# Optimization experiments

Measured on AMD Instinct MI355X. Metric: run time of the kernel, lower is better.

Reference implementation:

```python
import jax, jax.numpy as jnp
import numpy as np

SHAPE = (16, 1, 64, 128, 128)  # volume exactly equals the NCC window [64,128,128]
WIN_SIZE = 64.0 * 128.0 * 128.0


def setup_inputs() -> dict:
    key = jax.random.key(0)
    k1, k2, k3, k4 = jax.random.split(key, 4)
    out = jax.random.uniform(k1, SHAPE, dtype=jnp.float32)
    y_pred = jax.random.uniform(k2, SHAPE, dtype=jnp.float32)
    out_ccl = jax.random.randint(k3, SHAPE, 0, 2, dtype=jnp.int32)
    y_ccl = jax.random.randint(k4, SHAPE, 0, 2, dtype=jnp.int32)
    return {"out": out, "y_pred": y_pred, "out_ccl": out_ccl, "y_ccl": y_ccl}


def reference(out, y_pred, out_ccl, y_ccl):
    I, J = out, y_pred
    # masks at full resolution
    mask_I = jnp.where((out < 0.247) & (out_ccl > 0), 0.0, 1.0).astype(I.dtype)
    mask_J = jnp.where((y_pred < 0.247) & (y_ccl > 0), 0.0, 1.0).astype(J.dtype)

    # conv3d with an all-ones [64,128,128] kernel, stride 1, pad 0 over a
    # 64x128x128 volume == global sum per volume (output spatial dims are 1).
    ax = (2, 3, 4)
    I_sum = jnp.sum(I, axis=ax, keepdims=True)          # [B,1,1,1,1]
    J_sum = jnp.sum(J, axis=ax, keepdims=True)
    I2_sum = jnp.sum(I * I, axis=ax, keepdims=True)
    J2_sum = jnp.sum(J * J, axis=ax, keepdims=True)
    IJ_sum = jnp.sum(I * J, axis=ax, keepdims=True)

    u_I = I_sum / WIN_SIZE
    u_J = J_sum / WIN_SIZE
    cross = IJ_sum - u_J * I_sum - u_I * J_sum + u_I * u_J * WIN_SIZE
    I_var = I2_sum - 2.0 * u_I * I_sum + u_I * u_I * WIN_SIZE
    J_var = J2_sum - 2.0 * u_J * J_sum + u_J * u_J * WIN_SIZE
    cc = cross * cross / (I_var * J_var + 1e-5)         # [B,1,1,1,1]

    # broadcast per-volume cc against full-resolution masks, then mean
    return jnp.mean(-cc * mask_J * mask_I)
```

## Files before the change

### kernel.cpp

```cpp
#include <hip/hip_runtime.h>


#define NB   16
#define VOL  (64 * 128 * 128)
#define BPB  256
#define TPB  256
#define EPT  16

__device__ __forceinline__ double wave_reduce(double v) {
    #pragma unroll
    for (int off = 32; off > 0; off >>= 1) v += __shfl_down(v, off, 64);
    return v;
}

__global__ __launch_bounds__(TPB) void ncc_partial(
    const float* __restrict__ I, const float* __restrict__ J,
    const int* __restrict__ CI, const int* __restrict__ CJ,
    double* __restrict__ part)
{
    const int b = blockIdx.y;
    const size_t base = (size_t)b * VOL + (size_t)blockIdx.x * (TPB * EPT);
    const int tid = threadIdx.x;

    const float4* I4 = reinterpret_cast<const float4*>(I + base);
    const float4* J4 = reinterpret_cast<const float4*>(J + base);
    const int4*   C4 = reinterpret_cast<const int4*>(CI + base);
    const int4*   D4 = reinterpret_cast<const int4*>(CJ + base);

    double sI = 0.0, sJ = 0.0, sI2 = 0.0, sJ2 = 0.0, sIJ = 0.0;
    int cnt = 0;

    #pragma unroll
    for (int k = 0; k < EPT / 4; ++k) {
        const int idx = tid + k * TPB;
        float4 iv = I4[idx];
        float4 jv = J4[idx];
        int4   cv = C4[idx];
        int4   dv = D4[idx];

        float fi[4] = {iv.x, iv.y, iv.z, iv.w};
        float fj[4] = {jv.x, jv.y, jv.z, jv.w};
        int   ki[4] = {cv.x, cv.y, cv.z, cv.w};
        int   kj[4] = {dv.x, dv.y, dv.z, dv.w};

        #pragma unroll
        for (int e = 0; e < 4; ++e) {
            double di = (double)fi[e];
            double dj = (double)fj[e];
            sI += di;
            sJ += dj;
            sI2 = fma(di, di, sI2);
            sJ2 = fma(dj, dj, sJ2);
            sIJ = fma(di, dj, sIJ);
            bool zI = (di < 0.247) && (ki[e] > 0);
            bool zJ = (dj < 0.247) && (kj[e] > 0);
            cnt += (!zI && !zJ) ? 1 : 0;
        }
    }

    double v[6] = {sI, sJ, sI2, sJ2, sIJ, (double)cnt};
    #pragma unroll
    for (int q = 0; q < 6; ++q) v[q] = wave_reduce(v[q]);

    __shared__ double sh[TPB / 64][6];
    const int wave = tid >> 6, lane = tid & 63;
    if (lane == 0) {
        #pragma unroll
        for (int q = 0; q < 6; ++q) sh[wave][q] = v[q];
    }
    __syncthreads();

    if (tid == 0) {
        double o[6] = {0, 0, 0, 0, 0, 0};
        for (int w = 0; w < TPB / 64; ++w)
            for (int q = 0; q < 6; ++q) o[q] += sh[w][q];
        double* p = part + ((size_t)b * BPB + blockIdx.x) * 6;
        #pragma unroll
        for (int q = 0; q < 6; ++q) p[q] = o[q];
    }
}

__global__ __launch_bounds__(TPB) void ncc_final(
    const double* __restrict__ part, float* __restrict__ outp)
{
    const int tid = threadIdx.x;
    __shared__ double sh[TPB / 64][6];
    double total = 0.0;

    for (int b = 0; b < NB; ++b) {
        const double* p = part + ((size_t)b * BPB + tid) * 6;
        double v[6];
        #pragma unroll
        for (int q = 0; q < 6; ++q) v[q] = p[q];
        #pragma unroll
        for (int q = 0; q < 6; ++q) v[q] = wave_reduce(v[q]);

        const int wave = tid >> 6, lane = tid & 63;
        if (lane == 0) {
            #pragma unroll
            for (int q = 0; q < 6; ++q) sh[wave][q] = v[q];
        }
        __syncthreads();

        if (tid == 0) {
            double o[6] = {0, 0, 0, 0, 0, 0};
            for (int w = 0; w < TPB / 64; ++w)
                for (int q = 0; q < 6; ++q) o[q] += sh[w][q];
            const double W = (double)VOL;
            double uI = o[0] / W, uJ = o[1] / W;
            double cross = o[4] - uJ * o[0] - uI * o[1] + uI * uJ * W;
            double Ivar  = o[2] - 2.0 * uI * o[0] + uI * uI * W;
            double Jvar  = o[3] - 2.0 * uJ * o[1] + uJ * uJ * W;
            double cc = (cross * cross) / (Ivar * Jvar + 1e-5);
            total += -cc * o[5];
        }
        __syncthreads();
    }

    if (tid == 0) outp[0] = (float)(total / ((double)NB * (double)VOL));
}

extern "C" void kernel_launch(void* const* d_in, const int* in_sizes, int n_in,
                              void* d_out, int out_size, void* d_ws, size_t ws_size,
                              hipStream_t stream)
{
    const float* I  = (const float*)d_in[0];
    const float* J  = (const float*)d_in[1];
    const int*   CI = (const int*)d_in[2];
    const int*   CJ = (const int*)d_in[3];
    double* part = (double*)d_ws;

    dim3 grid(BPB, NB);
    ncc_partial<<<grid, TPB, 0, stream>>>(I, J, CI, CJ, part);
    ncc_final<<<1, TPB, 0, stream>>>(part, (float*)d_out);
}
```

Before: 259.3 us.

## Accumulate per-thread sums in float, hoist loads, parallelize final reduction

Per-thread accumulation of the five moment sums switches from double to float, with conversion to double only before the wave reduction. A float threshold equivalent to the double comparison against 0.247 is used for the mask test. All 16 vector loads are issued up front, and the partials are stored in struct-of-arrays layout. The final reduction now uses 1024 threads, one wave per volume, in place of a serial loop over volumes with barriers. FP64 work and the serialized tail are reduced, at some cost in precision for the 16-element per-thread sums.

```diff
diff --git a/kernel.cpp b/kernel.cpp
--- a/kernel.cpp
+++ b/kernel.cpp
@@ -6,11 +6,18 @@
 #define BPB  256
 #define TPB  256
 #define EPT  16
+#define NBLK (NB * BPB)
 
 __device__ __forceinline__ double wave_reduce(double v) {
     #pragma unroll
     for (int off = 32; off > 0; off >>= 1) v += __shfl_down(v, off, 64);
     return v;
+}
+
+__device__ __forceinline__ float mask_thresh() {
+    const float c = 0.247f;
+    if ((double)c < 0.247) return __uint_as_float(__float_as_uint(c) + 1u);
+    return c;
 }
 
 __global__ __launch_bounds__(TPB) void ncc_partial(
@@ -22,43 +29,46 @@
     const size_t base = (size_t)b * VOL + (size_t)blockIdx.x * (TPB * EPT);
     const int tid = threadIdx.x;
 
-    const float4* I4 = reinterpret_cast<const float4*>(I + base);
-    const float4* J4 = reinterpret_cast<const float4*>(J + base);
-    const int4*   C4 = reinterpret_cast<const int4*>(CI + base);
-    const int4*   D4 = reinterpret_cast<const int4*>(CJ + base);
+    const float4* __restrict__ I4 = reinterpret_cast<const float4*>(I + base);
+    const float4* __restrict__ J4 = reinterpret_cast<const float4*>(J + base);
+    const int4*   __restrict__ C4 = reinterpret_cast<const int4*>(CI + base);
+    const int4*   __restrict__ D4 = reinterpret_cast<const int4*>(CJ + base);
 
-    double sI = 0.0, sJ = 0.0, sI2 = 0.0, sJ2 = 0.0, sIJ = 0.0;
+    float4 iv[4]; float4 jv[4]; int4 cv[4]; int4 dv[4];
+    #pragma unroll
+    for (int k = 0; k < 4; ++k) iv[k] = I4[tid + k * TPB];
+    #pragma unroll
+    for (int k = 0; k < 4; ++k) jv[k] = J4[tid + k * TPB];
+    #pragma unroll
+    for (int k = 0; k < 4; ++k) cv[k] = C4[tid + k * TPB];
+    #pragma unroll
+    for (int k = 0; k < 4; ++k) dv[k] = D4[tid + k * TPB];
+
+    const float TH = mask_thresh();
+    float sI = 0.f, sJ = 0.f, sI2 = 0.f, sJ2 = 0.f, sIJ = 0.f;
     int cnt = 0;
 
     #pragma unroll
-    for (int k = 0; k < EPT / 4; ++k) {
-        const int idx = tid + k * TPB;
-        float4 iv = I4[idx];
-        float4 jv = J4[idx];
-        int4   cv = C4[idx];
-        int4   dv = D4[idx];
-
-        float fi[4] = {iv.x, iv.y, iv.z, iv.w};
-        float fj[4] = {jv.x, jv.y, jv.z, jv.w};
-        int   ki[4] = {cv.x, cv.y, cv.z, cv.w};
-        int   kj[4] = {dv.x, dv.y, dv.z, dv.w};
-
+    for (int k = 0; k < 4; ++k) {
+        float fi[4] = {iv[k].x, iv[k].y, iv[k].z, iv[k].w};
+        float fj[4] = {jv[k].x, jv[k].y, jv[k].z, jv[k].w};
+        int   ki[4] = {cv[k].x, cv[k].y, cv[k].z, cv[k].w};
+        int   kj[4] = {dv[k].x, dv[k].y, dv[k].z, dv[k].w};
         #pragma unroll
         for (int e = 0; e < 4; ++e) {
-            double di = (double)fi[e];
-            double dj = (double)fj[e];
-            sI += di;
-            sJ += dj;
-            sI2 = fma(di, di, sI2);
-            sJ2 = fma(dj, dj, sJ2);
-            sIJ = fma(di, dj, sIJ);
-            bool zI = (di < 0.247) && (ki[e] > 0);
-            bool zJ = (dj < 0.247) && (kj[e] > 0);
+            sI += fi[e];
+            sJ += fj[e];
+            sI2 = fmaf(fi[e], fi[e], sI2);
+            sJ2 = fmaf(fj[e], fj[e], sJ2);
+            sIJ = fmaf(fi[e], fj[e], sIJ);
+            bool zI = (fi[e] < TH) && (ki[e] > 0);
+            bool zJ = (fj[e] < TH) && (kj[e] > 0);
             cnt += (!zI && !zJ) ? 1 : 0;
         }
     }
 
-    double v[6] = {sI, sJ, sI2, sJ2, sIJ, (double)cnt};
+    double v[6] = {(double)sI, (double)sJ, (double)sI2,
+                   (double)sJ2, (double)sIJ, (double)cnt};
     #pragma unroll
     for (int q = 0; q < 6; ++q) v[q] = wave_reduce(v[q]);
 
@@ -71,53 +81,50 @@
     __syncthreads();
 
     if (tid == 0) {
-        double o[6] = {0, 0, 0, 0, 0, 0};
-        for (int w = 0; w < TPB / 64; ++w)
-            for (int q = 0; q < 6; ++q) o[q] += sh[w][q];
-        double* p = part + ((size_t)b * BPB + blockIdx.x) * 6;
+        const int gb = b * BPB + blockIdx.x;
         #pragma unroll
-        for (int q = 0; q < 6; ++q) p[q] = o[q];
+        for (int q = 0; q < 6; ++q) {
+            double o = 0.0;
+            for (int w = 0; w < TPB / 64; ++w) o += sh[w][q];
+            part[(size_t)q * NBLK + gb] = o;
+        }
     }
 }
 
-__global__ __launch_bounds__(TPB) void ncc_final(
+__global__ __launch_bounds__(1024) void ncc_final(
     const double* __restrict__ part, float* __restrict__ outp)
 {
     const int tid = threadIdx.x;
-    __shared__ double sh[TPB / 64][6];
-    double total = 0.0;
+    const int w = tid >> 6;
+    const int l = tid & 63;
 
-    for (int b = 0; b < NB; ++b) {
-        const double* p = part + ((size_t)b * BPB + tid) * 6;
-        double v[6];
+    double v[6] = {0, 0, 0, 0, 0, 0};
+    #pragma unroll
+    for (int k = 0; k < BPB / 64; ++k) {
+        const int p = w * BPB + k * 64 + l;
         #pragma unroll
-        for (int q = 0; q < 6; ++q) v[q] = p[q];
-        #pragma unroll
-        for (int q = 0; q < 6; ++q) v[q] = wave_reduce(v[q]);
+        for (int q = 0; q < 6; ++q) v[q] += part[(size_t)q * NBLK + p];
+    }
+    #pragma unroll
+    for (int q = 0; q < 6; ++q) v[q] = wave_reduce(v[q]);
 
-        const int wave = tid >> 6, lane = tid & 63;
-        if (lane == 0) {
-            #pragma unroll
-            for (int q = 0; q < 6; ++q) sh[wave][q] = v[q];
-        }
-        __syncthreads();
+    __shared__ double acc[NB];
+    if (l == 0) {
+        const double W = (double)VOL;
+        double uI = v[0] / W, uJ = v[1] / W;
+        double cross = v[4] - uJ * v[0] - uI * v[1] + uI * uJ * W;
+        double Ivar  = v[2] - 2.0 * uI * v[0] + uI * uI * W;
+        double Jvar  = v[3] - 2.0 * uJ * v[1] + uJ * uJ * W;
+        double cc = (cross * cross) / (Ivar * Jvar + 1e-5);
+        acc[w] = -cc * v[5];
+    }
+    __syncthreads();
 
-        if (tid == 0) {
-            double o[6] = {0, 0, 0, 0, 0, 0};
-            for (int w = 0; w < TPB / 64; ++w)
-                for (int q = 0; q < 6; ++q) o[q] += sh[w][q];
-            const double W = (double)VOL;
-            double uI = o[0] / W, uJ = o[1] / W;
-            double cross = o[4] - uJ * o[0] - uI * o[1] + uI * uJ * W;
-            double Ivar  = o[2] - 2.0 * uI * o[0] + uI * uI * W;
-            double Jvar  = o[3] - 2.0 * uJ * o[1] + uJ * uJ * W;
-            double cc = (cross * cross) / (Ivar * Jvar + 1e-5);
-            total += -cc * o[5];
-        }
-        __syncthreads();
+    if (tid == 0) {
+        double t = 0.0;
+        for (int b = 0; b < NB; ++b) t += acc[b];
+        outp[0] = (float)(t / ((double)NB * (double)VOL));
     }
-
-    if (tid == 0) outp[0] = (float)(total / ((double)NB * (double)VOL));
 }
 
 extern "C" void kernel_launch(void* const* d_in, const int* in_sizes, int n_in,
@@ -132,5 +139,5 @@
 
     dim3 grid(BPB, NB);
     ncc_partial<<<grid, TPB, 0, stream>>>(I, J, CI, CJ, part);
-    ncc_final<<<1, TPB, 0, stream>>>(part, (float*)d_out);
+    ncc_final<<<1, 1024, 0, stream>>>(part, (float*)d_out);
 }
```

Result: faster. 240.4 us (-7.3%).
